# Optimization experiments

Hardware: AMD Instinct MI355X
Metric: run time of the kernel (lower is better)

## Reference

```python
import jax, jax.numpy as jnp
import numpy as np

N, IN_DIM, OUT_DIM = 8192, 128, 64
ALPHA = 0.2  # LeakyReLU negative slope
NEG_INF = -1e12


def setup_inputs() -> dict:
    key = jax.random.key(0)
    k1, k2, k3, k4 = jax.random.split(key, 4)
    x = jax.random.normal(k1, (N, IN_DIM), dtype=jnp.float32)
    adj = jax.random.randint(k2, (N, N), 0, 2, dtype=jnp.int32)
    W = jax.random.normal(k3, (IN_DIM, OUT_DIM), dtype=jnp.float32) * 0.1
    a = jax.random.normal(k4, (2 * OUT_DIM, 1), dtype=jnp.float32) * 0.1
    return {"x": x, "adj": adj, "W": W, "a": a}


def reference(x, adj, W, a):
    Wh = x @ W                                   # [N, out_dim]
    Wh1 = Wh @ a[:OUT_DIM, :]                    # [N, 1] source scores
    Wh2 = Wh @ a[OUT_DIM:, :]                    # [N, 1] target scores
    e = Wh1 + Wh2.T                              # [N, N] additive attention
    e = jnp.where(e > 0, e, ALPHA * e)           # LeakyReLU
    scores = jnp.where(adj > 0, e, NEG_INF)      # mask non-edges
    attention = jax.nn.softmax(scores, axis=1)   # row-wise softmax
    h_prime = attention @ Wh                     # [N, out_dim]
    return jax.nn.elu(h_prime)
```

## Files before the change

kernel.cpp:

```cpp
#include <hip/hip_runtime.h>


#define N 8192
#define IN_DIM 128
#define OUT_DIM 64
#define ALPHA 0.2f
#define LOG2E 1.44269504088896f
#define JC 16
#define CW (N / JC)
#define TW 64
#define NT (CW / TW)
#define LDP 72

typedef _Float16 half8 __attribute__((ext_vector_type(8)));
typedef _Float16 h2 __attribute__((ext_vector_type(2)));
typedef float f32x4 __attribute__((ext_vector_type(4)));

__global__ __launch_bounds__(64) void wh_kernel(
    const float* __restrict__ x, const float* __restrict__ W,
    const float* __restrict__ a, _Float16* __restrict__ Wh_t,
    float* __restrict__ s1L, float* __restrict__ s2L) {
  __shared__ float xs[IN_DIM];
  const int i = blockIdx.x;
  const int t = threadIdx.x;

  xs[t]      = x[(size_t)i * IN_DIM + t];
  xs[t + 64] = x[(size_t)i * IN_DIM + 64 + t];
  __syncthreads();

  float wh = 0.f;
#pragma unroll
  for (int d = 0; d < IN_DIM; ++d) wh = fmaf(xs[d], W[d * OUT_DIM + t], wh);

  Wh_t[(size_t)t * N + i] = (_Float16)wh;

  float p1 = wh * a[t];
  float p2 = wh * a[64 + t];
#pragma unroll
  for (int off = 32; off; off >>= 1) {
    p1 += __shfl_down(p1, off);
    p2 += __shfl_down(p2, off);
  }
  if (t == 0) {
    s1L[i] = p1 * LOG2E;
    s2L[i] = p2 * LOG2E;
  }
}

__global__ __launch_bounds__(256) void max_kernel(
    const float* __restrict__ s1L, const float* __restrict__ s2L,
    float* __restrict__ mm) {
  __shared__ float red[8];
  const int t = threadIdx.x;
  float m1 = -1e30f, m2 = -1e30f;
  for (int idx = t; idx < N; idx += 256) {
    m1 = fmaxf(m1, s1L[idx]);
    m2 = fmaxf(m2, s2L[idx]);
  }
#pragma unroll
  for (int off = 32; off; off >>= 1) {
    m1 = fmaxf(m1, __shfl_down(m1, off));
    m2 = fmaxf(m2, __shfl_down(m2, off));
  }
  if ((t & 63) == 0) {
    red[t >> 6] = m1;
    red[4 + (t >> 6)] = m2;
  }
  __syncthreads();
  if (t == 0) {
    m1 = fmaxf(fmaxf(red[0], red[1]), fmaxf(red[2], red[3]));
    m2 = fmaxf(fmaxf(red[4], red[5]), fmaxf(red[6], red[7]));
    float e = m1 + m2;
    mm[0] = m1;
    mm[1] = fmaxf(e, ALPHA * e);
  }
}

__global__ __launch_bounds__(256) void ftab_kernel(
    const float* __restrict__ s1L, const float* __restrict__ s2L,
    const float* __restrict__ mm, unsigned int* __restrict__ Fi,
    _Float16* __restrict__ TTh) {
  const int j = blockIdx.x * 256 + threadIdx.x;
  const float m1 = mm[0], ML = mm[1];

  const _Float16 f1 = (_Float16)exp2f(s1L[j] - m1);
  const _Float16 f2 = (_Float16)exp2f(0.2f * (s1L[j] - m1));
  h2 f;
  f[0] = f1;
  f[1] = f2;
  Fi[j] = __builtin_bit_cast(unsigned int, f);

  TTh[(j >> 2) * 8 + (j & 3)]     = (_Float16)exp2f(s2L[j] - (ML - m1));
  TTh[(j >> 2) * 8 + 4 + (j & 3)] = (_Float16)exp2f(0.2f * s2L[j] - (ML - 0.2f * m1));
}

__global__ __launch_bounds__(256) void bpack_kernel(
    const _Float16* __restrict__ Wh_t, _Float16* __restrict__ Bpack) {
  const int kt = blockIdx.x;
  const int t = threadIdx.x;
  const int fg = t >> 6;
  const int lane = t & 63;
  const int q = (t >> 4) & 3;
  const int r16 = t & 15;
  const half8 v =
      *(const half8*)(Wh_t + (size_t)(fg * 16 + r16) * N + kt * 32 + q * 8);
  *(half8*)(Bpack + ((size_t)(kt * 4 + fg) * 64 + lane) * 8) = v;
}

__global__ __launch_bounds__(256, 4) void attn_kernel(
    const int* __restrict__ adj, const _Float16* __restrict__ Bpack,
    const unsigned int* __restrict__ Fi, const uint4* __restrict__ TT,
    float* __restrict__ accp, float* __restrict__ lp) {
  __shared__ __align__(16) _Float16 Ps[4 * 16 * LDP];

  const int t = threadIdx.x;
  const int w = t >> 6;
  const int lane = t & 63;
  const int q = lane >> 4;
  const int r16 = lane & 15;
  const int r4 = lane >> 4;
  const int l16 = lane & 15;
  const int rb = (int)(gridDim.x - 1 - blockIdx.x);
  const int i0 = rb * 64 + w * 16;
  const int c = blockIdx.y;
  const int jb = c * CW;

  h2 f1b[4], f2b[4];
#pragma unroll
  for (int it = 0; it < 4; ++it) {
    const unsigned int u = Fi[i0 + 4 * it + r4];
    f1b[it] = __builtin_bit_cast(h2, (u & 0xFFFFu) * 0x00010001u);
    f2b[it] = __builtin_bit_cast(h2, (u >> 16) * 0x00010001u);
  }

  half8 bones;
#pragma unroll
  for (int e = 0; e < 8; ++e)
    bones[e] = (r16 == 0) ? (_Float16)1.0f : (_Float16)0.0f;

  f32x4 acc[5] = {{0.f, 0.f, 0.f, 0.f}, {0.f, 0.f, 0.f, 0.f},
                  {0.f, 0.f, 0.f, 0.f}, {0.f, 0.f, 0.f, 0.f},
                  {0.f, 0.f, 0.f, 0.f}};

  const int* ap = adj + (size_t)(i0 + r4) * N + jb + l16 * 4;
  _Float16* Pw = Ps + w * 16 * LDP;
  const _Float16* ldA = Pw + r16 * LDP + q * 8;
  _Float16* stP = Pw + r4 * LDP + l16 * 4;

  int4 av[4];
#pragma unroll
  for (int it = 0; it < 4; ++it) av[it] = *(const int4*)(ap + it * 4 * N);
  uint4 tt = TT[(jb >> 2) + l16];

  for (int jt = 0; jt < NT; ++jt) {
    const int ktb = c * 16 + jt * 2;

    half8 bf[2][4];
#pragma unroll
    for (int ks = 0; ks < 2; ++ks)
#pragma unroll
      for (int fg = 0; fg < 4; ++fg)
        bf[ks][fg] = *(const half8*)(Bpack +
                                     ((size_t)((ktb + ks) * 4 + fg) * 64 + lane) * 8);

    const int jnoff = ((jt + 1) & (NT - 1)) * TW;
    int4 nav[4];
#pragma unroll
    for (int it = 0; it < 4; ++it)
      nav[it] = *(const int4*)(ap + jnoff + it * 4 * N);
    const uint4 ntt = TT[((jb + jnoff) >> 2) + l16];

#pragma unroll
    for (int it = 0; it < 4; ++it) {
      const unsigned int mlo =
          (unsigned int)(av[it].x | (av[it].y << 16)) * 0x3C00u;
      const unsigned int mhi =
          (unsigned int)(av[it].z | (av[it].w << 16)) * 0x3C00u;
      const h2 t1lo = __builtin_bit_cast(h2, tt.x);
      const h2 t1hi = __builtin_bit_cast(h2, tt.y);
      const h2 t2lo = __builtin_bit_cast(h2, tt.z);
      const h2 t2hi = __builtin_bit_cast(h2, tt.w);
      h2 plo = __builtin_elementwise_max(f1b[it] * t1lo, f2b[it] * t2lo) *
               __builtin_bit_cast(h2, mlo);
      h2 phi = __builtin_elementwise_max(f1b[it] * t1hi, f2b[it] * t2hi) *
               __builtin_bit_cast(h2, mhi);
      uint2 pw;
      pw.x = __builtin_bit_cast(unsigned int, plo);
      pw.y = __builtin_bit_cast(unsigned int, phi);
      *(uint2*)(stP + it * 4 * LDP) = pw;
    }

#pragma unroll
    for (int ks = 0; ks < 2; ++ks) {
      const half8 aF = *(const half8*)(ldA + ks * 32);
#pragma unroll
      for (int fg = 0; fg < 4; ++fg)
        acc[fg] =
            __builtin_amdgcn_mfma_f32_16x16x32_f16(aF, bf[ks][fg], acc[fg],
                                                   0, 0, 0);
      acc[4] =
          __builtin_amdgcn_mfma_f32_16x16x32_f16(aF, bones, acc[4], 0, 0, 0);
    }

#pragma unroll
    for (int it = 0; it < 4; ++it) av[it] = nav[it];
    tt = ntt;
  }

#pragma unroll
  for (int fg = 0; fg < 4; ++fg) {
#pragma unroll
    for (int r = 0; r < 4; ++r) {
      accp[((size_t)c * N + i0 + q * 4 + r) * OUT_DIM + fg * 16 + r16] =
          acc[fg][r];
    }
  }
  if (r16 == 0) {
#pragma unroll
    for (int r = 0; r < 4; ++r) lp[(size_t)c * N + i0 + q * 4 + r] = acc[4][r];
  }
}

__global__ __launch_bounds__(256) void reduce_kernel(
    const float* __restrict__ accp, const float* __restrict__ lp,
    float* __restrict__ out) {
  const int tid = blockIdx.x * 256 + threadIdx.x;
  const int i = tid >> 6;
  float s = 0.f, l = 0.f;
#pragma unroll
  for (int c = 0; c < JC; ++c) s += accp[(size_t)c * N * OUT_DIM + tid];
#pragma unroll
  for (int c = 0; c < JC; ++c) l += lp[(size_t)c * N + i];
  float v = s / l;
  out[tid] = v > 0.f ? v : expm1f(v);
}

extern "C" void kernel_launch(void* const* d_in, const int* in_sizes, int n_in,
                              void* d_out, int out_size, void* d_ws,
                              size_t ws_size, hipStream_t stream) {
  const float* x = (const float*)d_in[0];
  const int* adj = (const int*)d_in[1];
  const float* W = (const float*)d_in[2];
  const float* a = (const float*)d_in[3];
  float* out = (float*)d_out;

  char* ws = (char*)d_ws;
  _Float16* Wh_t = (_Float16*)ws;
  float* s1L = (float*)(ws + (1u << 20));
  float* s2L = s1L + N;
  float* mm = s2L + N;
  _Float16* Bpack = (_Float16*)(ws + (2u << 20));
  unsigned int* Fi = (unsigned int*)(ws + (3u << 20));
  _Float16* TTh = (_Float16*)(ws + (3u << 20) + (512u << 10));
  float* accp = (float*)(ws + (4u << 20));
  float* lp = accp + (size_t)JC * N * OUT_DIM;

  wh_kernel<<<N, 64, 0, stream>>>(x, W, a, Wh_t, s1L, s2L);
  max_kernel<<<1, 256, 0, stream>>>(s1L, s2L, mm);
  ftab_kernel<<<N / 256, 256, 0, stream>>>(s1L, s2L, mm, Fi, TTh);
  bpack_kernel<<<N / 32, 256, 0, stream>>>(Wh_t, Bpack);
  attn_kernel<<<dim3(N / 64, JC), 256, 0, stream>>>(
      adj, Bpack, Fi, (const uint4*)TTh, accp, lp);
  reduce_kernel<<<N * OUT_DIM / 256, 256, 0, stream>>>(accp, lp, out);
}
```

Measured before the change: 429.1 us.

## Widen attention column tiles to 256 and halve column chunks

The attention kernel now processes 256-column tiles per iteration, with each lane loading 4 contiguous adjacency ints across the full 64-lane width, and splits the columns into 8 chunks instead of 16. This halves the partial-sum traffic to the reduce step. Row factors are broadcast with shuffles, and B fragments are loaded inside the MFMA loop instead of being prefetched. The explicit software prefetch of the next adjacency tile and the reversed block order are dropped, so memory-latency hiding now depends on occupancy. The grid is also halved, which may reduce parallelism.

```diff
diff --git a/kernel.cpp b/kernel.cpp
--- a/kernel.cpp
+++ b/kernel.cpp
@@ -6,15 +6,16 @@
 #define OUT_DIM 64
 #define ALPHA 0.2f
 #define LOG2E 1.44269504088896f
-#define JC 16
-#define CW (N / JC)
-#define TW 64
-#define NT (CW / TW)
-#define LDP 72
+#define JC 8
+#define LDP 264
 
 typedef _Float16 half8 __attribute__((ext_vector_type(8)));
 typedef _Float16 h2 __attribute__((ext_vector_type(2)));
 typedef float f32x4 __attribute__((ext_vector_type(4)));
+
+static __device__ __forceinline__ h2 bc_h2(unsigned u) {
+  return __builtin_bit_cast(h2, u);
+}
 
 __global__ __launch_bounds__(64) void wh_kernel(
     const float* __restrict__ x, const float* __restrict__ W,
@@ -83,15 +84,15 @@
   const int j = blockIdx.x * 256 + threadIdx.x;
   const float m1 = mm[0], ML = mm[1];
 
-  const _Float16 f1 = (_Float16)exp2f(s1L[j] - m1);
-  const _Float16 f2 = (_Float16)exp2f(0.2f * (s1L[j] - m1));
+  const float v1 = s1L[j] - m1;
   h2 f;
-  f[0] = f1;
-  f[1] = f2;
+  f[0] = (_Float16)exp2f(v1);
+  f[1] = (_Float16)exp2f(0.2f * v1);
   Fi[j] = __builtin_bit_cast(unsigned int, f);
 
   TTh[(j >> 2) * 8 + (j & 3)]     = (_Float16)exp2f(s2L[j] - (ML - m1));
-  TTh[(j >> 2) * 8 + 4 + (j & 3)] = (_Float16)exp2f(0.2f * s2L[j] - (ML - 0.2f * m1));
+  TTh[(j >> 2) * 8 + 4 + (j & 3)] =
+      (_Float16)exp2f(0.2f * s2L[j] - (ML - 0.2f * m1));
 }
 
 __global__ __launch_bounds__(256) void bpack_kernel(
@@ -118,93 +119,70 @@
   const int lane = t & 63;
   const int q = lane >> 4;
   const int r16 = lane & 15;
-  const int r4 = lane >> 4;
-  const int l16 = lane & 15;
-  const int rb = (int)(gridDim.x - 1 - blockIdx.x);
-  const int i0 = rb * 64 + w * 16;
+  const int i0 = blockIdx.x * 64 + w * 16;
   const int c = blockIdx.y;
-  const int jb = c * CW;
-
-  h2 f1b[4], f2b[4];
-#pragma unroll
-  for (int it = 0; it < 4; ++it) {
-    const unsigned int u = Fi[i0 + 4 * it + r4];
-    f1b[it] = __builtin_bit_cast(h2, (u & 0xFFFFu) * 0x00010001u);
-    f2b[it] = __builtin_bit_cast(h2, (u >> 16) * 0x00010001u);
-  }
+  const int jb = c * (N / JC);
+
+  _Float16* Pw = Ps + w * 16 * LDP;
+  const _Float16* ldA = Pw + r16 * LDP + q * 8;
 
   half8 bones;
 #pragma unroll
   for (int e = 0; e < 8; ++e)
     bones[e] = (r16 == 0) ? (_Float16)1.0f : (_Float16)0.0f;
+
+  const unsigned fi_all = Fi[i0 + r16];
+  const int* apb = adj + (size_t)i0 * N + jb + lane * 4;
+  const uint4* ttb = TT + (jb >> 2) + lane;
 
   f32x4 acc[5] = {{0.f, 0.f, 0.f, 0.f}, {0.f, 0.f, 0.f, 0.f},
                   {0.f, 0.f, 0.f, 0.f}, {0.f, 0.f, 0.f, 0.f},
                   {0.f, 0.f, 0.f, 0.f}};
 
-  const int* ap = adj + (size_t)(i0 + r4) * N + jb + l16 * 4;
-  _Float16* Pw = Ps + w * 16 * LDP;
-  const _Float16* ldA = Pw + r16 * LDP + q * 8;
-  _Float16* stP = Pw + r4 * LDP + l16 * 4;
-
-  int4 av[4];
-#pragma unroll
-  for (int it = 0; it < 4; ++it) av[it] = *(const int4*)(ap + it * 4 * N);
-  uint4 tt = TT[(jb >> 2) + l16];
-
-  for (int jt = 0; jt < NT; ++jt) {
-    const int ktb = c * 16 + jt * 2;
-
-    half8 bf[2][4];
-#pragma unroll
-    for (int ks = 0; ks < 2; ++ks)
-#pragma unroll
-      for (int fg = 0; fg < 4; ++fg)
-        bf[ks][fg] = *(const half8*)(Bpack +
-                                     ((size_t)((ktb + ks) * 4 + fg) * 64 + lane) * 8);
-
-    const int jnoff = ((jt + 1) & (NT - 1)) * TW;
-    int4 nav[4];
-#pragma unroll
-    for (int it = 0; it < 4; ++it)
-      nav[it] = *(const int4*)(ap + jnoff + it * 4 * N);
-    const uint4 ntt = TT[((jb + jnoff) >> 2) + l16];
-
-#pragma unroll
-    for (int it = 0; it < 4; ++it) {
-      const unsigned int mlo =
-          (unsigned int)(av[it].x | (av[it].y << 16)) * 0x3C00u;
-      const unsigned int mhi =
-          (unsigned int)(av[it].z | (av[it].w << 16)) * 0x3C00u;
-      const h2 t1lo = __builtin_bit_cast(h2, tt.x);
-      const h2 t1hi = __builtin_bit_cast(h2, tt.y);
-      const h2 t2lo = __builtin_bit_cast(h2, tt.z);
-      const h2 t2hi = __builtin_bit_cast(h2, tt.w);
-      h2 plo = __builtin_elementwise_max(f1b[it] * t1lo, f2b[it] * t2lo) *
-               __builtin_bit_cast(h2, mlo);
-      h2 phi = __builtin_elementwise_max(f1b[it] * t1hi, f2b[it] * t2hi) *
-               __builtin_bit_cast(h2, mhi);
-      uint2 pw;
-      pw.x = __builtin_bit_cast(unsigned int, plo);
-      pw.y = __builtin_bit_cast(unsigned int, phi);
-      *(uint2*)(stP + it * 4 * LDP) = pw;
+  for (int jt = 0; jt < 4; ++jt) {
+    const uint4 tt = ttb[jt * 64];
+
+#pragma unroll
+    for (int b = 0; b < 4; ++b) {
+      int4 av[4];
+#pragma unroll
+      for (int rr = 0; rr < 4; ++rr)
+        av[rr] = *(const int4*)(apb + (size_t)(b * 4 + rr) * N + jt * 256);
+#pragma unroll
+      for (int rr = 0; rr < 4; ++rr) {
+        const int row = b * 4 + rr;
+        const unsigned u = __shfl(fi_all, row);
+        const h2 f1 = bc_h2((u & 0xFFFFu) * 0x00010001u);
+        const h2 f2 = bc_h2((u >> 16) * 0x00010001u);
+        const unsigned mlo = (unsigned)(av[rr].x | (av[rr].y << 16)) * 0x3C00u;
+        const unsigned mhi = (unsigned)(av[rr].z | (av[rr].w << 16)) * 0x3C00u;
+        const h2 plo =
+            __builtin_elementwise_max(f1 * bc_h2(tt.x), f2 * bc_h2(tt.z)) *
+            bc_h2(mlo);
+        const h2 phi =
+            __builtin_elementwise_max(f1 * bc_h2(tt.y), f2 * bc_h2(tt.w)) *
+            bc_h2(mhi);
+        uint2 pw;
+        pw.x = __builtin_bit_cast(unsigned, plo);
+        pw.y = __builtin_bit_cast(unsigned, phi);
+        *(uint2*)(Pw + row * LDP + lane * 4) = pw;
+      }
     }
 
-#pragma unroll
-    for (int ks = 0; ks < 2; ++ks) {
+    const int ktb = c * 32 + jt * 8;
+#pragma unroll
+    for (int ks = 0; ks < 8; ++ks) {
       const half8 aF = *(const half8*)(ldA + ks * 32);
-#pragma unroll
-      for (int fg = 0; fg < 4; ++fg)
+      const _Float16* bp = Bpack + ((size_t)((ktb + ks) * 4) * 64 + lane) * 8;
+#pragma unroll
+      for (int fg = 0; fg < 4; ++fg) {
+        const half8 bf = *(const half8*)(bp + (size_t)fg * 512);
         acc[fg] =
-            __builtin_amdgcn_mfma_f32_16x16x32_f16(aF, bf[ks][fg], acc[fg],
-                                                   0, 0, 0);
+            __builtin_amdgcn_mfma_f32_16x16x32_f16(aF, bf, acc[fg], 0, 0, 0);
+      }
       acc[4] =
           __builtin_amdgcn_mfma_f32_16x16x32_f16(aF, bones, acc[4], 0, 0, 0);
     }
-
-#pragma unroll
-    for (int it = 0; it < 4; ++it) av[it] = nav[it];
-    tt = ntt;
   }
 
 #pragma unroll
@@ -247,13 +225,13 @@
   char* ws = (char*)d_ws;
   _Float16* Wh_t = (_Float16*)ws;
   float* s1L = (float*)(ws + (1u << 20));
-  float* s2L = s1L + N;
-  float* mm = s2L + N;
+  float* s2L = (float*)(ws + (1u << 20) + (64u << 10));
+  float* mm = (float*)(ws + (1u << 20) + (128u << 10));
+  unsigned* Fi = (unsigned*)(ws + (1u << 20) + (192u << 10));
+  _Float16* TTh = (_Float16*)(ws + (1u << 20) + (256u << 10));
   _Float16* Bpack = (_Float16*)(ws + (2u << 20));
-  unsigned int* Fi = (unsigned int*)(ws + (3u << 20));
-  _Float16* TTh = (_Float16*)(ws + (3u << 20) + (512u << 10));
   float* accp = (float*)(ws + (4u << 20));
-  float* lp = accp + (size_t)JC * N * OUT_DIM;
+  float* lp = (float*)(ws + (20u << 20));
 
   wh_kernel<<<N, 64, 0, stream>>>(x, W, a, Wh_t, s1L, s2L);
   max_kernel<<<1, 256, 0, stream>>>(s1L, s2L, mm);
```

Result: no change. 426.5 us (-0.6%).
